# Kernel optimization log

Measured on AMD Instinct MI355X. Metric: run time of the kernel, lower is better.

The kernel has to match this reference:

```python
import jax, jax.numpy as jnp
import numpy as np

TEMPERATURE = 0.07
BASE_TEMPERATURE = 0.07


def setup_inputs() -> dict:
    key = jax.random.key(0)
    k1, k2 = jax.random.split(key)
    features = jax.random.normal(k1, (4096, 2, 128), dtype=jnp.float32)
    labels = jax.random.randint(k2, (4096,), 0, 100, dtype=jnp.int64)
    return {"features": features, "labels": labels}


def reference(features, labels):
    # features: [B, n_views, D], labels: [B]
    B, n_views, D = features.shape
    N = B * n_views

    # label equality mask [B, B]
    lab = labels.reshape(-1, 1)
    mask = (lab == lab.T).astype(jnp.float32)

    # flatten views (C-order, same as torch .view) and L2-normalize
    feat = features.reshape(N, D)
    feat = feat / jnp.clip(jnp.linalg.norm(feat, axis=1, keepdims=True), 1e-12)

    # similarity logits [N, N]
    logits = jnp.matmul(feat, feat.T) / TEMPERATURE
    logits_max = jax.lax.stop_gradient(jnp.max(logits, axis=1, keepdims=True))
    logits = logits - logits_max

    # tile mask to [N, N] (torch .repeat ordering) and remove self-contrast
    mask = jnp.tile(mask, (n_views, n_views))
    logits_mask = 1.0 - jnp.eye(N, dtype=jnp.float32)
    mask = mask * logits_mask

    exp_logits = jnp.exp(logits) * logits_mask
    log_prob = logits - jnp.log(jnp.sum(exp_logits, axis=1, keepdims=True) + 1e-12)

    mask_pos_pairs = jnp.clip(jnp.sum(mask, axis=1), 1.0)
    mean_log_prob_pos = jnp.sum(mask * log_prob, axis=1) / mask_pos_pairs

    loss = -(TEMPERATURE / BASE_TEMPERATURE) * mean_log_prob_pos
    return jnp.mean(loss.reshape(n_views, B))
```

## Files before the change

kernel.cpp:

```cpp
#include <hip/hip_runtime.h>
#include <hip/hip_bf16.h>
#include <math.h>

#define NB 4096
#define NN 8192
#define DD 128
#define NSPLIT 16
#define CHUNK 64
#define NCHUNK 8

constexpr float INV_T = 14.285714285714286f;
constexpr float EC1   = 20.609929155556620f;
constexpr float EC0   = -20.609929155556620f;
constexpr float LN2   = 0.6931471805599453f;

typedef __attribute__((ext_vector_type(8))) short bf16x8;
typedef __attribute__((ext_vector_type(4))) float f32x4;

__device__ __forceinline__ float bf2f(ushort u) {
    union { unsigned int i; float f; } v; v.i = ((unsigned int)u) << 16; return v.f;
}

__global__ __launch_bounds__(256) void k_norm(const float* __restrict__ feat,
                                              ushort* __restrict__ fb,
                                              float* __restrict__ selfdot) {
    const int r    = (blockIdx.x * 256 + threadIdx.x) >> 6;
    const int lane = threadIdx.x & 63;
    const float2 v = ((const float2*)(feat + (size_t)r * DD))[lane];
    float ss = v.x * v.x + v.y * v.y;
#pragma unroll
    for (int off = 1; off < 64; off <<= 1) ss += __shfl_xor(ss, off, 64);
    const float scale = 1.0f / fmaxf(sqrtf(ss), 1e-12f);
    __hip_bfloat162 h2;
    h2.x = __float2bfloat16(v.x * scale);
    h2.y = __float2bfloat16(v.y * scale);
    ((__hip_bfloat162*)(fb + (size_t)r * DD))[lane] = h2;
    const float xb = bf2f(((ushort2*)&h2)->x), yb = bf2f(((ushort2*)&h2)->y);
    float s2 = xb * xb + yb * yb;
#pragma unroll
    for (int off = 1; off < 64; off <<= 1) s2 += __shfl_xor(s2, off, 64);
    if (lane == 0) selfdot[r] = s2;
}

__device__ __forceinline__ void stage_chunk(const ushort* __restrict__ fb, ushort* sbuf,
                                            int jb, int w, int n15, int q) {
    const ushort* g = fb + (size_t)(jb + w * 16 + n15) * DD + q * 8;
#pragma unroll
    for (int kt = 0; kt < 4; ++kt)
        __builtin_amdgcn_global_load_lds(
            (const __attribute__((address_space(1))) void*)(g + kt * 32),
            (__attribute__((address_space(3))) void*)(sbuf + (w * 4 + kt) * 512),
            16, 0, 0);
}

__global__ __launch_bounds__(256, 4) void k_main(const ushort* __restrict__ fb,
                                                 const int* __restrict__ labels,
                                                 float* __restrict__ g_se,
                                                 float* __restrict__ g_ps,
                                                 float* __restrict__ g_ct) {
    __shared__ ushort sB[2][CHUNK * DD];
    __shared__ int slab[512];

    const int tid  = threadIdx.x;
    const int lane = tid & 63;
    const int w    = tid >> 6;
    const int rb   = blockIdx.x >> 4;
    const int js   = blockIdx.x & (NSPLIT - 1);
    const int i0   = rb * 128 + w * 32;
    const int jb0  = js * 512;
    const int q    = lane >> 4;
    const int n15  = lane & 15;

    slab[tid]       = labels[(jb0 + tid) & (NB - 1)];
    slab[tid + 256] = labels[(jb0 + tid + 256) & (NB - 1)];

    bf16x8 afrag[2][4];
#pragma unroll
    for (int tt = 0; tt < 2; ++tt) {
        const ushort* rp = fb + (size_t)(i0 + tt * 16 + n15) * DD + q * 8;
#pragma unroll
        for (int kt = 0; kt < 4; ++kt) afrag[tt][kt] = *(const bf16x8*)(rp + kt * 32);
    }
    int labi[8];
#pragma unroll
    for (int tt = 0; tt < 2; ++tt)
#pragma unroll
        for (int r = 0; r < 4; ++r)
            labi[tt * 4 + r] = labels[(i0 + tt * 16 + q * 4 + r) & (NB - 1)];

    float a_se[8] = {}, a_ps[8] = {}, a_ct[8] = {};

    stage_chunk(fb, &sB[0][0], jb0, w, n15, q);
    __syncthreads();

    for (int c = 0; c < NCHUNK; ++c) {
        if (c + 1 < NCHUNK)
            stage_chunk(fb, &sB[(c + 1) & 1][0], jb0 + (c + 1) * CHUNK, w, n15, q);
        const ushort* sb = &sB[c & 1][0];
        const int crel = c * CHUNK;
#pragma unroll
        for (int jt = 0; jt < 4; ++jt) {
            bf16x8 bf[4];
#pragma unroll
            for (int kt = 0; kt < 4; ++kt)
                bf[kt] = *(const bf16x8*)(sb + (jt * 4 + kt) * 512 + lane * 8);
            const int labj = slab[crel + jt * 16 + n15];
            f32x4 a0 = {0.f, 0.f, 0.f, 0.f}, a1 = {0.f, 0.f, 0.f, 0.f};
#pragma unroll
            for (int kt = 0; kt < 4; ++kt) {
                a0 = __builtin_amdgcn_mfma_f32_16x16x32_bf16(afrag[0][kt], bf[kt], a0, 0, 0, 0);
                a1 = __builtin_amdgcn_mfma_f32_16x16x32_bf16(afrag[1][kt], bf[kt], a1, 0, 0, 0);
            }
#pragma unroll
            for (int r = 0; r < 4; ++r) {
                const float d0 = a0[r], d1 = a1[r];
                a_se[r]     += __builtin_amdgcn_exp2f(fmaf(d0, EC1, EC0));
                a_se[4 + r] += __builtin_amdgcn_exp2f(fmaf(d1, EC1, EC0));
                const bool m0 = (labi[r] == labj), m1 = (labi[4 + r] == labj);
                a_ps[r]     += m0 ? d0 : 0.0f;
                a_ps[4 + r] += m1 ? d1 : 0.0f;
                a_ct[r]     += m0 ? 1.0f : 0.0f;
                a_ct[4 + r] += m1 ? 1.0f : 0.0f;
            }
        }
        __syncthreads();
    }

#pragma unroll
    for (int s = 0; s < 8; ++s) {
        float v1 = a_se[s], v2 = a_ps[s], v3 = a_ct[s];
#pragma unroll
        for (int off = 1; off < 16; off <<= 1) {
            v1 += __shfl_xor(v1, off, 64);
            v2 += __shfl_xor(v2, off, 64);
            v3 += __shfl_xor(v3, off, 64);
        }
        if (n15 == 0) {
            const int row = i0 + (s >> 2) * 16 + q * 4 + (s & 3);
            g_se[js * NN + row] = v1;
            g_ps[js * NN + row] = v2;
            g_ct[js * NN + row] = v3;
        }
    }
}

__global__ __launch_bounds__(256) void k_final(const float* __restrict__ g_se,
                                               const float* __restrict__ g_ps,
                                               const float* __restrict__ g_ct,
                                               const float* __restrict__ selfdot,
                                               float* __restrict__ out) {
    const int r = blockIdx.x * 256 + threadIdx.x;
    float se = 0.f, ps = 0.f, ct = 0.f;
#pragma unroll
    for (int t = 0; t < NSPLIT; ++t) {
        se += g_se[t * NN + r];
        ps += g_ps[t * NN + r];
        ct += g_ct[t * NN + r];
    }
    const float sd = selfdot[r];
    se -= __builtin_amdgcn_exp2f(fmaf(sd, EC1, EC0));
    ct -= 1.0f;
    const float possum = INV_T * (ps - sd - ct);
    const float lg  = __builtin_amdgcn_logf(se + 1e-12f) * LN2;
    const float mlpp = (possum - ct * lg) / fmaxf(ct, 1.0f);
    float v = -mlpp * (1.0f / (float)NN);
#pragma unroll
    for (int off = 1; off < 64; off <<= 1) v += __shfl_xor(v, off, 64);
    __shared__ float sred[4];
    if ((threadIdx.x & 63) == 0) sred[threadIdx.x >> 6] = v;
    __syncthreads();
    if (threadIdx.x == 0) atomicAdd(out, sred[0] + sred[1] + sred[2] + sred[3]);
}

extern "C" void kernel_launch(void* const* d_in, const int* in_sizes, int n_in,
                              void* d_out, int out_size, void* d_ws, size_t ws_size,
                              hipStream_t stream) {
    const float* feat = (const float*)d_in[0];
    const int* labels = (const int*)d_in[1];
    float* out        = (float*)d_out;
    char* ws          = (char*)d_ws;

    ushort* fb      = (ushort*)ws;
    float* g_se     = (float*)(ws + (size_t)2 * 1024 * 1024);
    float* g_ps     = g_se + NSPLIT * NN;
    float* g_ct     = g_ps + NSPLIT * NN;
    float* selfdot  = g_ct + NSPLIT * NN;

    hipMemsetAsync(out, 0, sizeof(float), stream);
    k_norm<<<NN / 4, 256, 0, stream>>>(feat, fb, selfdot);
    k_main<<<64 * NSPLIT, 256, 0, stream>>>(fb, labels, g_se, g_ps, g_ct);
    k_final<<<NN / 256, 256, 0, stream>>>(g_se, g_ps, g_ct, selfdot, out);
}
```

Measured before the change: 99.34 us.

## Fuse finalize into main kernel via atomics and double rows per wave

```diff
diff --git a/kernel.cpp b/kernel.cpp
--- a/kernel.cpp
+++ b/kernel.cpp
@@ -23,8 +23,14 @@
 
 __global__ __launch_bounds__(256) void k_norm(const float* __restrict__ feat,
                                               ushort* __restrict__ fb,
-                                              float* __restrict__ selfdot) {
-    const int r    = (blockIdx.x * 256 + threadIdx.x) >> 6;
+                                              float* __restrict__ selfdot,
+                                              float* __restrict__ zbase,
+                                              float* __restrict__ out) {
+    const int gid = blockIdx.x * 256 + threadIdx.x;
+    if (gid < 3 * NN + 32) zbase[gid] = 0.0f;
+    if (gid == 0) out[0] = 0.0f;
+
+    const int r    = gid >> 6;
     const int lane = threadIdx.x & 63;
     const float2 v = ((const float2*)(feat + (size_t)r * DD))[lane];
     float ss = v.x * v.x + v.y * v.y;
@@ -53,20 +59,25 @@
             16, 0, 0);
 }
 
-__global__ __launch_bounds__(256, 4) void k_main(const ushort* __restrict__ fb,
+__global__ __launch_bounds__(256, 2) void k_main(const ushort* __restrict__ fb,
                                                  const int* __restrict__ labels,
+                                                 const float* __restrict__ selfdot,
                                                  float* __restrict__ g_se,
                                                  float* __restrict__ g_ps,
-                                                 float* __restrict__ g_ct) {
+                                                 float* __restrict__ g_ct,
+                                                 int* __restrict__ cnt,
+                                                 float* __restrict__ out) {
     __shared__ ushort sB[2][CHUNK * DD];
     __shared__ int slab[512];
+    __shared__ int lastflag;
+    __shared__ float sred[4];
 
     const int tid  = threadIdx.x;
     const int lane = tid & 63;
     const int w    = tid >> 6;
     const int rb   = blockIdx.x >> 4;
     const int js   = blockIdx.x & (NSPLIT - 1);
-    const int i0   = rb * 128 + w * 32;
+    const int i0   = rb * 256 + w * 64;
     const int jb0  = js * 512;
     const int q    = lane >> 4;
     const int n15  = lane & 15;
@@ -74,21 +85,21 @@
     slab[tid]       = labels[(jb0 + tid) & (NB - 1)];
     slab[tid + 256] = labels[(jb0 + tid + 256) & (NB - 1)];
 
-    bf16x8 afrag[2][4];
+    bf16x8 afrag[4][4];
 #pragma unroll
-    for (int tt = 0; tt < 2; ++tt) {
+    for (int tt = 0; tt < 4; ++tt) {
         const ushort* rp = fb + (size_t)(i0 + tt * 16 + n15) * DD + q * 8;
 #pragma unroll
         for (int kt = 0; kt < 4; ++kt) afrag[tt][kt] = *(const bf16x8*)(rp + kt * 32);
     }
-    int labi[8];
+    int labi[16];
 #pragma unroll
-    for (int tt = 0; tt < 2; ++tt)
+    for (int tt = 0; tt < 4; ++tt)
 #pragma unroll
         for (int r = 0; r < 4; ++r)
             labi[tt * 4 + r] = labels[(i0 + tt * 16 + q * 4 + r) & (NB - 1)];
 
-    float a_se[8] = {}, a_ps[8] = {}, a_ct[8] = {};
+    float a_se[16] = {}, a_ps[16] = {}, a_ct[16] = {};
 
     stage_chunk(fb, &sB[0][0], jb0, w, n15, q);
     __syncthreads();
@@ -105,29 +116,30 @@
             for (int kt = 0; kt < 4; ++kt)
                 bf[kt] = *(const bf16x8*)(sb + (jt * 4 + kt) * 512 + lane * 8);
             const int labj = slab[crel + jt * 16 + n15];
-            f32x4 a0 = {0.f, 0.f, 0.f, 0.f}, a1 = {0.f, 0.f, 0.f, 0.f};
+            f32x4 acc[4];
 #pragma unroll
-            for (int kt = 0; kt < 4; ++kt) {
-                a0 = __builtin_amdgcn_mfma_f32_16x16x32_bf16(afrag[0][kt], bf[kt], a0, 0, 0, 0);
-                a1 = __builtin_amdgcn_mfma_f32_16x16x32_bf16(afrag[1][kt], bf[kt], a1, 0, 0, 0);
-            }
+            for (int tt = 0; tt < 4; ++tt) acc[tt] = (f32x4){0.f, 0.f, 0.f, 0.f};
 #pragma unroll
-            for (int r = 0; r < 4; ++r) {
-                const float d0 = a0[r], d1 = a1[r];
-                a_se[r]     += __builtin_amdgcn_exp2f(fmaf(d0, EC1, EC0));
-                a_se[4 + r] += __builtin_amdgcn_exp2f(fmaf(d1, EC1, EC0));
-                const bool m0 = (labi[r] == labj), m1 = (labi[4 + r] == labj);
-                a_ps[r]     += m0 ? d0 : 0.0f;
-                a_ps[4 + r] += m1 ? d1 : 0.0f;
-                a_ct[r]     += m0 ? 1.0f : 0.0f;
-                a_ct[4 + r] += m1 ? 1.0f : 0.0f;
-            }
+            for (int kt = 0; kt < 4; ++kt)
+#pragma unroll
+                for (int tt = 0; tt < 4; ++tt)
+                    acc[tt] = __builtin_amdgcn_mfma_f32_16x16x32_bf16(afrag[tt][kt], bf[kt], acc[tt], 0, 0, 0);
+#pragma unroll
+            for (int tt = 0; tt < 4; ++tt)
+#pragma unroll
+                for (int r = 0; r < 4; ++r) {
+                    const float d = acc[tt][r];
+                    a_se[tt * 4 + r] += __builtin_amdgcn_exp2f(fmaf(d, EC1, EC0));
+                    const bool m = (labi[tt * 4 + r] == labj);
+                    a_ps[tt * 4 + r] += m ? d : 0.0f;
+                    a_ct[tt * 4 + r] += m ? 1.0f : 0.0f;
+                }
         }
         __syncthreads();
     }
 
 #pragma unroll
-    for (int s = 0; s < 8; ++s) {
+    for (int s = 0; s < 16; ++s) {
         float v1 = a_se[s], v2 = a_ps[s], v3 = a_ct[s];
 #pragma unroll
         for (int off = 1; off < 16; off <<= 1) {
@@ -137,39 +149,33 @@
         }
         if (n15 == 0) {
             const int row = i0 + (s >> 2) * 16 + q * 4 + (s & 3);
-            g_se[js * NN + row] = v1;
-            g_ps[js * NN + row] = v2;
-            g_ct[js * NN + row] = v3;
+            atomicAdd(&g_se[row], v1);
+            atomicAdd(&g_ps[row], v2);
+            atomicAdd(&g_ct[row], v3);
         }
     }
-}
 
-__global__ __launch_bounds__(256) void k_final(const float* __restrict__ g_se,
-                                               const float* __restrict__ g_ps,
-                                               const float* __restrict__ g_ct,
-                                               const float* __restrict__ selfdot,
-                                               float* __restrict__ out) {
-    const int r = blockIdx.x * 256 + threadIdx.x;
-    float se = 0.f, ps = 0.f, ct = 0.f;
+    __syncthreads();
+    __threadfence();
+    if (tid == 0) lastflag = (atomicAdd(&cnt[rb], 1) == NSPLIT - 1);
+    __syncthreads();
+    if (lastflag) {
+        __threadfence();
+        const int r = rb * 256 + tid;
+        const float se0 = g_se[r], ps = g_ps[r], ct0 = g_ct[r];
+        const float sd  = selfdot[r];
+        const float se  = se0 - __builtin_amdgcn_exp2f(fmaf(sd, EC1, EC0));
+        const float ct  = ct0 - 1.0f;
+        const float possum = INV_T * (ps - sd - ct);
+        const float lg  = __builtin_amdgcn_logf(se + 1e-12f) * LN2;
+        const float mlpp = (possum - ct * lg) / fmaxf(ct, 1.0f);
+        float v = -mlpp * (1.0f / (float)NN);
 #pragma unroll
-    for (int t = 0; t < NSPLIT; ++t) {
-        se += g_se[t * NN + r];
-        ps += g_ps[t * NN + r];
-        ct += g_ct[t * NN + r];
+        for (int off = 1; off < 64; off <<= 1) v += __shfl_xor(v, off, 64);
+        if (lane == 0) sred[w] = v;
+        __syncthreads();
+        if (tid == 0) atomicAdd(out, sred[0] + sred[1] + sred[2] + sred[3]);
     }
-    const float sd = selfdot[r];
-    se -= __builtin_amdgcn_exp2f(fmaf(sd, EC1, EC0));
-    ct -= 1.0f;
-    const float possum = INV_T * (ps - sd - ct);
-    const float lg  = __builtin_amdgcn_logf(se + 1e-12f) * LN2;
-    const float mlpp = (possum - ct * lg) / fmaxf(ct, 1.0f);
-    float v = -mlpp * (1.0f / (float)NN);
-#pragma unroll
-    for (int off = 1; off < 64; off <<= 1) v += __shfl_xor(v, off, 64);
-    __shared__ float sred[4];
-    if ((threadIdx.x & 63) == 0) sred[threadIdx.x >> 6] = v;
-    __syncthreads();
-    if (threadIdx.x == 0) atomicAdd(out, sred[0] + sred[1] + sred[2] + sred[3]);
 }
 
 extern "C" void kernel_launch(void* const* d_in, const int* in_sizes, int n_in,
@@ -181,13 +187,12 @@
     char* ws          = (char*)d_ws;
 
     ushort* fb      = (ushort*)ws;
-    float* g_se     = (float*)(ws + (size_t)2 * 1024 * 1024);
-    float* g_ps     = g_se + NSPLIT * NN;
-    float* g_ct     = g_ps + NSPLIT * NN;
-    float* selfdot  = g_ct + NSPLIT * NN;
+    float* selfdot  = (float*)(ws + (size_t)2 * 1024 * 1024);
+    float* g_se     = selfdot + NN;
+    float* g_ps     = g_se + NN;
+    float* g_ct     = g_ps + NN;
+    int*   cnt      = (int*)(g_ct + NN);
 
-    hipMemsetAsync(out, 0, sizeof(float), stream);
-    k_norm<<<NN / 4, 256, 0, stream>>>(feat, fb, selfdot);
-    k_main<<<64 * NSPLIT, 256, 0, stream>>>(fb, labels, g_se, g_ps, g_ct);
-    k_final<<<NN / 256, 256, 0, stream>>>(g_se, g_ps, g_ct, selfdot, out);
+    k_norm<<<NN / 4, 256, 0, stream>>>(feat, fb, selfdot, g_se, out);
+    k_main<<<32 * NSPLIT, 256, 0, stream>>>(fb, labels, selfdot, g_se, g_ps, g_ct, cnt, out);
 }
```

Result: slower. 121.1 us (+21.9%).
